# Kernel optimization log

Hardware: AMD Instinct MI355X
Metric: run time of the kernel (lower is better)

Reference implementation:

```python
import jax, jax.numpy as jnp
import numpy as np

B, S, DIN, DOUT = 4, 2048, 4096, 4096

def setup_inputs() -> dict:
    key = jax.random.key(0)
    k1, k2, k3, k4 = jax.random.split(key, 4)
    x = jax.random.normal(k1, (B, S, DIN), dtype=jnp.float32)
    # symmetric int8 weight values in [-127, 127]
    quantized_weight = jax.random.randint(k2, (DOUT, DIN), -127, 128, dtype=jnp.int32).astype(jnp.int8)
    weight_scale = jax.random.uniform(k3, (), dtype=jnp.float32) * 0.01 + 1e-4
    bias = jax.random.normal(k4, (DOUT,), dtype=jnp.float32)
    return {"x": x, "quantized_weight": quantized_weight, "weight_scale": weight_scale, "bias": bias}

def reference(x, quantized_weight, weight_scale, bias) -> jnp.ndarray:
    # dequantize_tensor: (q.float() - 0) * scale
    weight_fp32 = quantized_weight.astype(jnp.float32) * weight_scale  # [DOUT, DIN]
    # nn.functional.linear: x @ W^T + b
    return jnp.einsum('bsi,oi->bso', x, weight_fp32) + bias
```

## Files before the change

### kernel.cpp

```cpp
#include <hip/hip_runtime.h>
#include <stdint.h>
#include <stddef.h>

constexpr int MDIM = 8192;
constexpr int NDIM = 4096;
constexpr int KDIM = 4096;

using f32x4 = __attribute__((ext_vector_type(4))) float;
using s16x4 = __attribute__((ext_vector_type(4))) short;
using s16x8 = __attribute__((ext_vector_type(8))) short;
using i32x4 = __attribute__((ext_vector_type(4))) int;

__device__ __forceinline__ short f32_to_bf16_rn(float f) {
  union { float f; uint32_t u; } v; v.f = f;
  uint32_t r = (v.u + 0x7FFFu + ((v.u >> 16) & 1u)) >> 16;
  return (short)(uint16_t)r;
}

__global__ void __launch_bounds__(256) quant_x_kernel(const float* __restrict__ in,
                                                      signed char* __restrict__ out,
                                                      float* __restrict__ sx) {
  const int row = blockIdx.x;
  const int t   = threadIdx.x;
  const float* rp = in + (size_t)row * KDIM;
  f32x4 v[4];
  float m = 0.0f;
#pragma unroll
  for (int j = 0; j < 4; ++j) {
    v[j] = *(const f32x4*)(rp + t * 16 + j * 4);
#pragma unroll
    for (int e = 0; e < 4; ++e) m = fmaxf(m, __builtin_fabsf(v[j][e]));
  }
#pragma unroll
  for (int off = 32; off > 0; off >>= 1) m = fmaxf(m, __shfl_xor(m, off, 64));
  __shared__ float wmax[4];
  const int wv = t >> 6, ln = t & 63;
  if (ln == 0) wmax[wv] = m;
  __syncthreads();
  m = fmaxf(fmaxf(wmax[0], wmax[1]), fmaxf(wmax[2], wmax[3]));
  const float inv = (m > 0.0f) ? (127.0f / m) : 0.0f;
  if (t == 0) sx[row] = m * (1.0f / 127.0f);
  i32x4 o;
#pragma unroll
  for (int j = 0; j < 4; ++j) {
    int b[4];
#pragma unroll
    for (int e = 0; e < 4; ++e) {
      int q = (int)rintf(v[j][e] * inv);
      q = q < -127 ? -127 : (q > 127 ? 127 : q);
      b[e] = q & 255;
    }
    o[j] = b[0] | (b[1] << 8) | (b[2] << 16) | (b[3] << 24);
  }
  *(i32x4*)(out + (size_t)row * KDIM + t * 16) = o;
}

__global__ void __launch_bounds__(256) quant_w_kernel(const int* __restrict__ in,
                                                      signed char* __restrict__ out, int n16) {
  int i = blockIdx.x * 256 + threadIdx.x;
  const int stride = gridDim.x * 256;
  for (; i < n16; i += stride) {
    const i32x4* p = (const i32x4*)(in + (size_t)i * 16);
    i32x4 o;
#pragma unroll
    for (int j = 0; j < 4; ++j) {
      i32x4 a = p[j];
      o[j] = (a[0] & 255) | ((a[1] & 255) << 8) | ((a[2] & 255) << 16) | ((a[3] & 255) << 24);
    }
    *(i32x4*)(out + (size_t)i * 16) = o;
  }
}


#define BAR asm volatile("s_barrier" ::: "memory")
#define WAITVM(n) asm volatile("s_waitcnt vmcnt(" #n ")" ::: "memory")

#define GLL(src, dst) __builtin_amdgcn_global_load_lds(                     \
    (const __attribute__((address_space(1))) void*)(src),                   \
    (__attribute__((address_space(3))) void*)(dst), 16, 0, 0)

#define STG4(grow, ldsmat, tau) do {                                        \
  const int buf_ = (tau) & 1;                                               \
  _Pragma("unroll") for (int h_ = 0; h_ < 2; ++h_)                          \
  _Pragma("unroll") for (int rh_ = 0; rh_ < 2; ++rh_)                       \
    GLL((grow) + (size_t)(rh_ * 128 + r0) * 4096 + (size_t)(tau) * 128      \
            + h_ * 64 + cb,                                                 \
        lds + (ldsmat) + buf_ * 32768 + h_ * 16384 + rh_ * 8192 + t * 16);  \
} while (0)

#define LDA8(bufc, fi, h) (*(const i32x4*)(lds + (bufc) * 32768             \
    + (h) * 16384 + wmoff + (fi) * 1024 + laneoff))
#define LDB8(bufc, fj, h) (*(const i32x4*)(lds + 65536 + (bufc) * 32768     \
    + (h) * 16384 + wnoff + (fj) * 1024 + laneoff))

#define MFMAQ(base, afr) do {                                               \
  __builtin_amdgcn_s_setprio(1);                                            \
  _Pragma("unroll") for (int i_ = 0; i_ < 4; ++i_)                          \
  _Pragma("unroll") for (int j_ = 0; j_ < 4; ++j_)                          \
    acc[(base) + i_][j_] = __builtin_amdgcn_mfma_i32_16x16x64_i8(           \
        afr[i_], bf[j_], acc[(base) + i_][j_], 0, 0, 0);                    \
  __builtin_amdgcn_s_setprio(0);                                            \
} while (0)

#define KT128(t_, cur, stg) do {                                            \
                                                   \
  _Pragma("unroll") for (int j_ = 0; j_ < 4; ++j_) bf[j_] = LDB8(cur, j_, 0); \
  _Pragma("unroll") for (int i_ = 0; i_ < 4; ++i_) af[i_] = LDA8(cur, i_, 0); \
  if (stg) STG4(Brow, 65536, (t_) + 1);                                     \
  BAR; MFMAQ(0, af); BAR;                                                   \
                                       \
  _Pragma("unroll") for (int i_ = 0; i_ < 4; ++i_) ag[i_] = LDA8(cur, 4 + i_, 0); \
  if (stg) STG4(Arow, 0, (t_) + 1);                                         \
  BAR; MFMAQ(4, ag); BAR;                                                   \
                                                   \
  _Pragma("unroll") for (int j_ = 0; j_ < 4; ++j_) bf[j_] = LDB8(cur, j_, 1); \
  _Pragma("unroll") for (int i_ = 0; i_ < 4; ++i_) af[i_] = LDA8(cur, i_, 1); \
  BAR; MFMAQ(0, af); BAR;                                                   \
                                                   \
  _Pragma("unroll") for (int i_ = 0; i_ < 4; ++i_) ag[i_] = LDA8(cur, 4 + i_, 1); \
  BAR; MFMAQ(4, ag);                                                        \
  if (stg) WAITVM(0);                                                       \
  BAR;                                                                      \
} while (0)

__global__ void __launch_bounds__(512, 2) gemm_i8_pipe(
    const signed char* __restrict__ A, const signed char* __restrict__ Bw,
    const float* __restrict__ sx, const float* __restrict__ scale_p,
    const float* __restrict__ bias, float* __restrict__ out) {
  __shared__ __align__(16) char lds[131072];

  const int t      = threadIdx.x;
  const int lane   = t & 63;
  const int wave   = t >> 6;
  const int wm     = wave >> 2;
  const int wn     = wave & 3;
  const int lane15 = lane & 15;
  const int lh     = lane >> 4;

  const int laneoff = (lane15 * 64 + lh * 16) ^ ((lane15 & 8) << 2);
  const int wmoff   = wm * 8192;
  const int wnoff   = wn * 4096;

  const int ax = ((t >> 5) & 1) << 5;
  const int a0 = (t * 16) ^ ax;
  const int r0 = a0 >> 6;
  const int cb = a0 & 63;

  const int bid   = blockIdx.x;
  const int wg    = (bid & 7) * 64 + (bid >> 3);
  const int ntile = wg & 15;
  const int mtile = wg >> 4;
  const int m0 = mtile * 256;
  const int n0 = ntile * 256;

  const char* Arow = (const char*)(A + (size_t)m0 * KDIM);
  const char* Brow = (const char*)(Bw + (size_t)n0 * KDIM);

  i32x4 acc[8][4] = {};
  i32x4 af[4], ag[4], bf[4];

  STG4(Brow, 65536, 0);
  STG4(Arow, 0,     0);
  WAITVM(0);
  BAR;

#pragma unroll 1
  for (int tp = 0; tp < 15; ++tp) {
    KT128(2 * tp,     0, 1);
    KT128(2 * tp + 1, 1, 1);
  }
  KT128(30, 0, 1);
  KT128(31, 1, 0);

  const float sw = scale_p[0];
  float bv[4];
#pragma unroll
  for (int j = 0; j < 4; ++j) bv[j] = bias[n0 + wn * 64 + j * 16 + lane15];
#pragma unroll
  for (int i = 0; i < 8; ++i) {
    const int rowb = m0 + wm * 128 + i * 16 + lh * 4;
    float sxq[4];
#pragma unroll
    for (int q = 0; q < 4; ++q) sxq[q] = sx[rowb + q] * sw;
#pragma unroll
    for (int j = 0; j < 4; ++j) {
      const int col = n0 + wn * 64 + j * 16 + lane15;
#pragma unroll
      for (int q = 0; q < 4; ++q)
        out[(size_t)(rowb + q) * NDIM + col] = (float)acc[i][j][q] * sxq[q] + bv[j];
    }
  }
}

constexpr int FTILE = 128;
constexpr int FBK   = 64;

__global__ void __launch_bounds__(256) gemm_raw(
    const float* __restrict__ X, const int* __restrict__ W,
    const float* __restrict__ scale_p, const float* __restrict__ bias,
    float* __restrict__ out) {
  __shared__ short As[FTILE * FBK];
  __shared__ short Bs[FTILE * FBK];

  const int t      = threadIdx.x;
  const int lane   = t & 63;
  const int wave   = t >> 6;
  const int wm     = wave >> 1;
  const int wn     = wave & 1;
  const int lane15   = lane & 15;
  const int laneHalf = lane >> 4;

  const int bid   = blockIdx.x;
  const int wg    = (bid & 7) * 256 + (bid >> 3);
  const int ntile = wg & 31;
  const int mtile = wg >> 5;
  const int m0 = mtile * FTILE;
  const int n0 = ntile * FTILE;

  f32x4 acc[4][4] = {};

  for (int k0 = 0; k0 < KDIM; k0 += FBK) {
    __syncthreads();
#pragma unroll
    for (int r = 0; r < 8; ++r) {
      const int f   = r * 256 + t;
      const int row = f >> 4;
      const int c4  = (f & 15) * 4;
      f32x4 v = *(const f32x4*)(X + (size_t)(m0 + row) * KDIM + (k0 + c4));
      s16x4 h;
#pragma unroll
      for (int j = 0; j < 4; ++j) h[j] = f32_to_bf16_rn(v[j]);
      *(s16x4*)&As[row * FBK + c4] = h;

      i32x4 wv = *(const i32x4*)(W + (size_t)(n0 + row) * KDIM + (k0 + c4));
      s16x4 hw;
#pragma unroll
      for (int j = 0; j < 4; ++j) hw[j] = f32_to_bf16_rn((float)wv[j]);
      *(s16x4*)&Bs[row * FBK + c4] = hw;
    }
    __syncthreads();

#pragma unroll
    for (int kk = 0; kk < FBK; kk += 32) {
      const int kb = kk + laneHalf * 8;
      s16x8 af[4], bf[4];
#pragma unroll
      for (int i = 0; i < 4; ++i) {
        af[i] = *(const s16x8*)&As[(wm * 64 + i * 16 + lane15) * FBK + kb];
        bf[i] = *(const s16x8*)&Bs[(wn * 64 + i * 16 + lane15) * FBK + kb];
      }
#pragma unroll
      for (int i = 0; i < 4; ++i)
#pragma unroll
        for (int j = 0; j < 4; ++j)
          acc[i][j] = __builtin_amdgcn_mfma_f32_16x16x32_bf16(af[i], bf[j], acc[i][j], 0, 0, 0);
    }
  }

  const float s = scale_p[0];
#pragma unroll
  for (int j = 0; j < 4; ++j) {
    const int col = n0 + wn * 64 + j * 16 + lane15;
    const float bv = bias[col];
#pragma unroll
    for (int i = 0; i < 4; ++i) {
      const int row = m0 + wm * 64 + i * 16 + laneHalf * 4;
#pragma unroll
      for (int q = 0; q < 4; ++q)
        out[(size_t)(row + q) * NDIM + col] = acc[i][j][q] * s + bv;
    }
  }
}

extern "C" void kernel_launch(void* const* d_in, const int* in_sizes, int n_in,
                              void* d_out, int out_size, void* d_ws, size_t ws_size,
                              hipStream_t stream) {
  const float* x     = (const float*)d_in[0];
  const int*   w     = (const int*)d_in[1];
  const float* scale = (const float*)d_in[2];
  const float* bias  = (const float*)d_in[3];
  float* out = (float*)d_out;

  const size_t a_bytes = (size_t)MDIM * KDIM;
  const size_t b_bytes = (size_t)NDIM * KDIM;
  const size_t need    = a_bytes + b_bytes + MDIM * 4;

  if (ws_size >= need) {
    signed char* Ai8 = (signed char*)d_ws;
    signed char* Bi8 = Ai8 + a_bytes;
    float*       sxp = (float*)(Bi8 + b_bytes);
    quant_x_kernel<<<MDIM, 256, 0, stream>>>(x, Ai8, sxp);
    quant_w_kernel<<<4096, 256, 0, stream>>>(w, Bi8, (int)(b_bytes / 16));
    const int nwg = (MDIM / 256) * (NDIM / 256);
    gemm_i8_pipe<<<nwg, 512, 0, stream>>>(Ai8, Bi8, sxp, scale, bias, out);
  } else {
    const int nwg = (MDIM / FTILE) * (NDIM / FTILE);
    gemm_raw<<<nwg, 256, 0, stream>>>(x, w, scale, bias, out);
  }
}
```

Measured before the change: 184.9 us.

## Stream A fragments from global into registers and ring-buffer B in LDS

Drops LDS staging for the activation matrix. Each wave now loads its A fragments straight from global memory into double-buffered registers, one 64-wide k step ahead. B is staged through a 4-slot LDS ring with 64-byte k steps, and there is a single barrier per step instead of the old multi-barrier 128-wide step. The aim is to cut LDS traffic and barriers, at the cost of the four N-waves redundantly loading the same A rows from global/L2 with strided 16-byte accesses. Occupancy also drops to one 512-thread block per CU.

```diff
diff --git a/kernel.cpp b/kernel.cpp
--- a/kernel.cpp
+++ b/kernel.cpp
@@ -79,55 +79,44 @@
     (const __attribute__((address_space(1))) void*)(src),                   \
     (__attribute__((address_space(3))) void*)(dst), 16, 0, 0)
 
-#define STG4(grow, ldsmat, tau) do {                                        \
-  const int buf_ = (tau) & 1;                                               \
-  _Pragma("unroll") for (int h_ = 0; h_ < 2; ++h_)                          \
-  _Pragma("unroll") for (int rh_ = 0; rh_ < 2; ++rh_)                       \
-    GLL((grow) + (size_t)(rh_ * 128 + r0) * 4096 + (size_t)(tau) * 128      \
-            + h_ * 64 + cb,                                                 \
-        lds + (ldsmat) + buf_ * 32768 + h_ * 16384 + rh_ * 8192 + t * 16);  \
+#define STGB_PRO(tau) do {                                                  \
+  GLL(Brow + (size_t)r0 * 4096 + (tau) * 64 + cb,                           \
+      lds + (tau) * 16384 + t * 16);                                        \
+  GLL(Brow + (size_t)(128 + r0) * 4096 + (tau) * 64 + cb,                   \
+      lds + (tau) * 16384 + 8192 + t * 16);                                 \
 } while (0)
 
-#define LDA8(bufc, fi, h) (*(const i32x4*)(lds + (bufc) * 32768             \
-    + (h) * 16384 + wmoff + (fi) * 1024 + laneoff))
-#define LDB8(bufc, fj, h) (*(const i32x4*)(lds + 65536 + (bufc) * 32768     \
-    + (h) * 16384 + wnoff + (fj) * 1024 + laneoff))
-
-#define MFMAQ(base, afr) do {                                               \
+#define STGB_LOOP(ub) do {                                                  \
+  GLL(Bpt + (size_t)r0 * 4096 + 192 + cb,                                   \
+      lds + (ub) * 16384 + t * 16);                                         \
+  GLL(Bpt + (size_t)(128 + r0) * 4096 + 192 + cb,                           \
+      lds + (ub) * 16384 + 8192 + t * 16);                                  \
+} while (0)
+
+#define LDBF(u, j) (*(const i32x4*)(lds + (u) * 16384 + wnoff + (j) * 1024 + laneoff))
+
+#define KTF(u, AFC, AFN, dostg, doaf) do {                                  \
+  _Pragma("unroll") for (int j_ = 0; j_ < 4; ++j_) bf[j_] = LDBF(u, j_);    \
+  if (doaf) {                                                               \
+    _Pragma("unroll") for (int i_ = 0; i_ < 8; ++i_)                        \
+      AFN[i_] = *(const i32x4*)(Apt + (size_t)i_ * 65536 + 64);             \
+  }                                                                         \
+  if (dostg) STGB_LOOP(((u) + 3) & 3);                                      \
   __builtin_amdgcn_s_setprio(1);                                            \
-  _Pragma("unroll") for (int i_ = 0; i_ < 4; ++i_)                          \
+  _Pragma("unroll") for (int i_ = 0; i_ < 8; ++i_)                          \
   _Pragma("unroll") for (int j_ = 0; j_ < 4; ++j_)                          \
-    acc[(base) + i_][j_] = __builtin_amdgcn_mfma_i32_16x16x64_i8(           \
-        afr[i_], bf[j_], acc[(base) + i_][j_], 0, 0, 0);                    \
+    acc[i_][j_] = __builtin_amdgcn_mfma_i32_16x16x64_i8(                    \
+        AFC[i_], bf[j_], acc[i_][j_], 0, 0, 0);                             \
   __builtin_amdgcn_s_setprio(0);                                            \
+  BAR;                                                                      \
+  Apt += 64; Bpt += 64;                                                     \
 } while (0)
 
-#define KT128(t_, cur, stg) do {                                            \
-                                                   \
-  _Pragma("unroll") for (int j_ = 0; j_ < 4; ++j_) bf[j_] = LDB8(cur, j_, 0); \
-  _Pragma("unroll") for (int i_ = 0; i_ < 4; ++i_) af[i_] = LDA8(cur, i_, 0); \
-  if (stg) STG4(Brow, 65536, (t_) + 1);                                     \
-  BAR; MFMAQ(0, af); BAR;                                                   \
-                                       \
-  _Pragma("unroll") for (int i_ = 0; i_ < 4; ++i_) ag[i_] = LDA8(cur, 4 + i_, 0); \
-  if (stg) STG4(Arow, 0, (t_) + 1);                                         \
-  BAR; MFMAQ(4, ag); BAR;                                                   \
-                                                   \
-  _Pragma("unroll") for (int j_ = 0; j_ < 4; ++j_) bf[j_] = LDB8(cur, j_, 1); \
-  _Pragma("unroll") for (int i_ = 0; i_ < 4; ++i_) af[i_] = LDA8(cur, i_, 1); \
-  BAR; MFMAQ(0, af); BAR;                                                   \
-                                                   \
-  _Pragma("unroll") for (int i_ = 0; i_ < 4; ++i_) ag[i_] = LDA8(cur, 4 + i_, 1); \
-  BAR; MFMAQ(4, ag);                                                        \
-  if (stg) WAITVM(0);                                                       \
-  BAR;                                                                      \
-} while (0)
-
-__global__ void __launch_bounds__(512, 2) gemm_i8_pipe(
+__global__ void __launch_bounds__(512, 1) gemm_i8_flat(
     const signed char* __restrict__ A, const signed char* __restrict__ Bw,
     const float* __restrict__ sx, const float* __restrict__ scale_p,
     const float* __restrict__ bias, float* __restrict__ out) {
-  __shared__ __align__(16) char lds[131072];
+  __shared__ __align__(16) char lds[65536];
 
   const int t      = threadIdx.x;
   const int lane   = t & 63;
@@ -138,7 +127,6 @@
   const int lh     = lane >> 4;
 
   const int laneoff = (lane15 * 64 + lh * 16) ^ ((lane15 & 8) << 2);
-  const int wmoff   = wm * 8192;
   const int wnoff   = wn * 4096;
 
   const int ax = ((t >> 5) & 1) << 5;
@@ -153,24 +141,32 @@
   const int m0 = mtile * 256;
   const int n0 = ntile * 256;
 
-  const char* Arow = (const char*)(A + (size_t)m0 * KDIM);
   const char* Brow = (const char*)(Bw + (size_t)n0 * KDIM);
+  const char* Bpt  = Brow;
+  const signed char* Apt = A + (size_t)(m0 + wm * 128 + lane15) * KDIM + lh * 16;
 
   i32x4 acc[8][4] = {};
-  i32x4 af[4], ag[4], bf[4];
-
-  STG4(Brow, 65536, 0);
-  STG4(Arow, 0,     0);
+  i32x4 afE[8], afO[8], bf[4];
+
+  STGB_PRO(0);
+  STGB_PRO(1);
+  STGB_PRO(2);
   WAITVM(0);
   BAR;
+#pragma unroll
+  for (int i_ = 0; i_ < 8; ++i_) afE[i_] = *(const i32x4*)(Apt + (size_t)i_ * 65536);
 
 #pragma unroll 1
   for (int tp = 0; tp < 15; ++tp) {
-    KT128(2 * tp,     0, 1);
-    KT128(2 * tp + 1, 1, 1);
-  }
-  KT128(30, 0, 1);
-  KT128(31, 1, 0);
+    KTF(0, afE, afO, 1, 1);
+    KTF(1, afO, afE, 1, 1);
+    KTF(2, afE, afO, 1, 1);
+    KTF(3, afO, afE, 1, 1);
+  }
+  KTF(0, afE, afO, 1, 1);
+  KTF(1, afO, afE, 0, 1);
+  KTF(2, afE, afO, 0, 1);
+  KTF(3, afO, afE, 0, 0);
 
   const float sw = scale_p[0];
   float bv[4];
@@ -292,7 +288,7 @@
     quant_x_kernel<<<MDIM, 256, 0, stream>>>(x, Ai8, sxp);
     quant_w_kernel<<<4096, 256, 0, stream>>>(w, Bi8, (int)(b_bytes / 16));
     const int nwg = (MDIM / 256) * (NDIM / 256);
-    gemm_i8_pipe<<<nwg, 512, 0, stream>>>(Ai8, Bi8, sxp, scale, bias, out);
+    gemm_i8_flat<<<nwg, 512, 0, stream>>>(Ai8, Bi8, sxp, scale, bias, out);
   } else {
     const int nwg = (MDIM / FTILE) * (NDIM / FTILE);
     gemm_raw<<<nwg, 256, 0, stream>>>(x, w, scale, bias, out);
```

Measured after the change: 352.2 us. 90.5% more time.

## Deepen int8 GEMM prefetch to stage half-tiles two iterations ahead

Applied to the files above, without the earlier changes.

The int8 MFMA GEMM now issues global-to-LDS loads in finer half-K chunks spread over the four phases of each k-tile, prefetching up to two tiles ahead instead of one. The end-of-tile wait becomes vmcnt(6) rather than a full drain, so loads stay in flight across barriers. The LDS row mapping is also changed so each wave reads contiguous fragments under a new swizzle. The aim is to hide global memory latency behind MFMA work, but the buffer reuse ordering is fragile and a wrong count or race would corrupt data.

```diff
diff --git a/kernel.cpp b/kernel.cpp
--- a/kernel.cpp
+++ b/kernel.cpp
@@ -8,7 +8,6 @@
 
 using f32x4 = __attribute__((ext_vector_type(4))) float;
 using s16x4 = __attribute__((ext_vector_type(4))) short;
-using s16x8 = __attribute__((ext_vector_type(8))) short;
 using i32x4 = __attribute__((ext_vector_type(4))) int;
 
 __device__ __forceinline__ short f32_to_bf16_rn(float f) {
@@ -73,57 +72,64 @@
 
 
 #define BAR asm volatile("s_barrier" ::: "memory")
-#define WAITVM(n) asm volatile("s_waitcnt vmcnt(" #n ")" ::: "memory")
+#define WAITVM6 asm volatile("s_waitcnt vmcnt(6)" ::: "memory")
+#define WAITVM0 asm volatile("s_waitcnt vmcnt(0)" ::: "memory")
 
 #define GLL(src, dst) __builtin_amdgcn_global_load_lds(                     \
     (const __attribute__((address_space(1))) void*)(src),                   \
     (__attribute__((address_space(3))) void*)(dst), 16, 0, 0)
 
-#define STG4(grow, ldsmat, tau) do {                                        \
+#define STAGE(grow, ldsmat, ks, tau) do {                                   \
   const int buf_ = (tau) & 1;                                               \
-  _Pragma("unroll") for (int h_ = 0; h_ < 2; ++h_)                          \
-  _Pragma("unroll") for (int rh_ = 0; rh_ < 2; ++rh_)                       \
-    GLL((grow) + (size_t)(rh_ * 128 + r0) * 4096 + (size_t)(tau) * 128      \
-            + h_ * 64 + cb,                                                 \
-        lds + (ldsmat) + buf_ * 32768 + h_ * 16384 + rh_ * 8192 + t * 16);  \
-} while (0)
-
-#define LDA8(bufc, fi, h) (*(const i32x4*)(lds + (bufc) * 32768             \
-    + (h) * 16384 + wmoff + (fi) * 1024 + laneoff))
-#define LDB8(bufc, fj, h) (*(const i32x4*)(lds + 65536 + (bufc) * 32768     \
-    + (h) * 16384 + wnoff + (fj) * 1024 + laneoff))
-
-#define MFMAQ(base, afr) do {                                               \
+  GLL((grow) + (size_t)r0 * 4096 + (size_t)(tau) * 128 + (ks) * 64 + cb,    \
+      lds + (ldsmat) + buf_ * 32768 + (ks) * 16384 + t * 16);               \
+  GLL((grow) + (size_t)r1 * 4096 + (size_t)(tau) * 128 + (ks) * 64 + cb,    \
+      lds + (ldsmat) + buf_ * 32768 + (ks) * 16384 + 8192 + t * 16);        \
+} while (0)
+
+#define LDA(cur, ks, i) (*(const i32x4*)(lds + (cur) * 32768 + (ks) * 16384 \
+    + (wm * 8 + (i)) * 1024 + laneoff))
+#define LDB(cur, ks, j) (*(const i32x4*)(lds + 65536 + (cur) * 32768        \
+    + (ks) * 16384 + (wn * 4 + (j)) * 1024 + laneoff))
+
+#define READ_B(cur, ks) do {                                                \
+  _Pragma("unroll") for (int j = 0; j < 4; ++j) bf[j] = LDB(cur, ks, j);    \
+} while (0)
+#define READ_A(cur, ks, ibase) do {                                         \
+  _Pragma("unroll") for (int i = 0; i < 4; ++i) af[i] = LDA(cur, ks, (ibase) + i); \
+} while (0)
+
+#define MFMA16(ibase) do {                                                  \
   __builtin_amdgcn_s_setprio(1);                                            \
-  _Pragma("unroll") for (int i_ = 0; i_ < 4; ++i_)                          \
-  _Pragma("unroll") for (int j_ = 0; j_ < 4; ++j_)                          \
-    acc[(base) + i_][j_] = __builtin_amdgcn_mfma_i32_16x16x64_i8(           \
-        afr[i_], bf[j_], acc[(base) + i_][j_], 0, 0, 0);                    \
+  _Pragma("unroll") for (int i = 0; i < 4; ++i)                             \
+  _Pragma("unroll") for (int j = 0; j < 4; ++j)                             \
+    acc[(ibase) + i][j] = __builtin_amdgcn_mfma_i32_16x16x64_i8(            \
+        af[i], bf[j], acc[(ibase) + i][j], 0, 0, 0);                        \
   __builtin_amdgcn_s_setprio(0);                                            \
 } while (0)
 
-#define KT128(t_, cur, stg) do {                                            \
+#define KTILE(t_, cur, nstage, endvm) do {                                  \
                                                    \
-  _Pragma("unroll") for (int j_ = 0; j_ < 4; ++j_) bf[j_] = LDB8(cur, j_, 0); \
-  _Pragma("unroll") for (int i_ = 0; i_ < 4; ++i_) af[i_] = LDA8(cur, i_, 0); \
-  if (stg) STG4(Brow, 65536, (t_) + 1);                                     \
-  BAR; MFMAQ(0, af); BAR;                                                   \
-                                       \
-  _Pragma("unroll") for (int i_ = 0; i_ < 4; ++i_) ag[i_] = LDA8(cur, 4 + i_, 0); \
-  if (stg) STG4(Arow, 0, (t_) + 1);                                         \
-  BAR; MFMAQ(4, ag); BAR;                                                   \
+  READ_B(cur, 0); READ_A(cur, 0, 0);                                        \
+  if ((nstage) >= 1) STAGE(Arow, 0, 1, (t_) + 1);        \
+  BAR; MFMA16(0); BAR;                                                      \
+                                        \
+  READ_A(cur, 0, 4);                                                        \
+  if ((nstage) == 4) STAGE(Brow, 65536, 0, (t_) + 2);    \
+  BAR; MFMA16(4); BAR;                                                      \
                                                    \
-  _Pragma("unroll") for (int j_ = 0; j_ < 4; ++j_) bf[j_] = LDB8(cur, j_, 1); \
-  _Pragma("unroll") for (int i_ = 0; i_ < 4; ++i_) af[i_] = LDA8(cur, i_, 1); \
-  BAR; MFMAQ(0, af); BAR;                                                   \
+  READ_B(cur, 1); READ_A(cur, 1, 0);                                        \
+  if ((nstage) == 4) STAGE(Arow, 0, 0, (t_) + 2);        \
+  BAR; MFMA16(0); BAR;                                                      \
                                                    \
-  _Pragma("unroll") for (int i_ = 0; i_ < 4; ++i_) ag[i_] = LDA8(cur, 4 + i_, 1); \
-  BAR; MFMAQ(4, ag);                                                        \
-  if (stg) WAITVM(0);                                                       \
+  READ_A(cur, 1, 4);                                                        \
+  if ((nstage) == 4) STAGE(Brow, 65536, 1, (t_) + 2);    \
+  BAR; MFMA16(4);                                                           \
+  if ((endvm) == 6) { WAITVM6; } else if ((endvm) == 0) { WAITVM0; }        \
   BAR;                                                                      \
 } while (0)
 
-__global__ void __launch_bounds__(512, 2) gemm_i8_pipe(
+__global__ void __launch_bounds__(512, 2) gemm_i8_8ph(
     const signed char* __restrict__ A, const signed char* __restrict__ Bw,
     const float* __restrict__ sx, const float* __restrict__ scale_p,
     const float* __restrict__ bias, float* __restrict__ out) {
@@ -138,12 +144,12 @@
   const int lh     = lane >> 4;
 
   const int laneoff = (lane15 * 64 + lh * 16) ^ ((lane15 & 8) << 2);
-  const int wmoff   = wm * 8192;
-  const int wnoff   = wn * 4096;
 
   const int ax = ((t >> 5) & 1) << 5;
   const int a0 = (t * 16) ^ ax;
-  const int r0 = a0 >> 6;
+  const int a1 = (8192 + t * 16) ^ ax;
+  const int r0 = (((a0 >> 10) & 15) << 4) | ((a0 >> 6) & 15);
+  const int r1 = (((a1 >> 10) & 15) << 4) | ((a1 >> 6) & 15);
   const int cb = a0 & 63;
 
   const int bid   = blockIdx.x;
@@ -157,20 +163,26 @@
   const char* Brow = (const char*)(Bw + (size_t)n0 * KDIM);
 
   i32x4 acc[8][4] = {};
-  i32x4 af[4], ag[4], bf[4];
-
-  STG4(Brow, 65536, 0);
-  STG4(Arow, 0,     0);
-  WAITVM(0);
+  i32x4 af[4], bf[4];
+
+  STAGE(Brow, 65536, 0, 0);
+  STAGE(Arow, 0,     0, 0);
+  STAGE(Brow, 65536, 1, 0);
+  STAGE(Arow, 0,     1, 0);
+  STAGE(Brow, 65536, 0, 1);
+  STAGE(Arow, 0,     0, 1);
+  STAGE(Brow, 65536, 1, 1);
+  WAITVM6;
   BAR;
 
 #pragma unroll 1
   for (int tp = 0; tp < 15; ++tp) {
-    KT128(2 * tp,     0, 1);
-    KT128(2 * tp + 1, 1, 1);
-  }
-  KT128(30, 0, 1);
-  KT128(31, 1, 0);
+    const int t2 = tp * 2;
+    KTILE(t2,     0, 4, 6);
+    KTILE(t2 + 1, 1, 4, 6);
+  }
+  KTILE(30, 0, 1, 0);
+  KTILE(31, 1, 0, -1);
 
   const float sw = scale_p[0];
   float bv[4];
@@ -243,11 +255,12 @@
 #pragma unroll
     for (int kk = 0; kk < FBK; kk += 32) {
       const int kb = kk + laneHalf * 8;
-      s16x8 af[4], bf[4];
+      using s16x8f = __attribute__((ext_vector_type(8))) short;
+      s16x8f af[4], bf[4];
 #pragma unroll
       for (int i = 0; i < 4; ++i) {
-        af[i] = *(const s16x8*)&As[(wm * 64 + i * 16 + lane15) * FBK + kb];
-        bf[i] = *(const s16x8*)&Bs[(wn * 64 + i * 16 + lane15) * FBK + kb];
+        af[i] = *(const s16x8f*)&As[(wm * 64 + i * 16 + lane15) * FBK + kb];
+        bf[i] = *(const s16x8f*)&Bs[(wn * 64 + i * 16 + lane15) * FBK + kb];
       }
 #pragma unroll
       for (int i = 0; i < 4; ++i)
@@ -292,7 +305,7 @@
     quant_x_kernel<<<MDIM, 256, 0, stream>>>(x, Ai8, sxp);
     quant_w_kernel<<<4096, 256, 0, stream>>>(w, Bi8, (int)(b_bytes / 16));
     const int nwg = (MDIM / 256) * (NDIM / 256);
-    gemm_i8_pipe<<<nwg, 512, 0, stream>>>(Ai8, Bi8, sxp, scale, bias, out);
+    gemm_i8_8ph<<<nwg, 512, 0, stream>>>(Ai8, Bi8, sxp, scale, bias, out);
   } else {
     const int nwg = (MDIM / FTILE) * (NDIM / FTILE);
     gemm_raw<<<nwg, 256, 0, stream>>>(x, w, scale, bias, out);
```

New measurement: 185.6 us. About the same (+0.4%).
